# Performance work log

Measured on AMD Instinct MI355X. Metric: run time of the kernel, lower is better.

## Reference

```python
import jax, jax.numpy as jnp
import numpy as np

IN_FEATURES = 4096
OUT_FEATURES = 11008
BATCH = 64


def setup_inputs() -> dict:
    key = jax.random.key(0)
    k_x, k_w, k_s, k_b = jax.random.split(key, 4)
    x = jax.random.normal(k_x, (BATCH, IN_FEATURES), dtype=jnp.float32)
    # int8-range quantized weights stored as int8 (symmetric, [-128, 127])
    weight_q = jax.random.randint(k_w, (OUT_FEATURES, IN_FEATURES), -128, 128, dtype=jnp.int8)
    # per-output-row scales, strictly positive (absmax/127 style)
    scale = jax.random.uniform(k_s, (OUT_FEATURES, 1), dtype=jnp.float32, minval=1e-4, maxval=2e-2)
    bias = jax.random.normal(k_b, (OUT_FEATURES,), dtype=jnp.float32)
    return {"x": x, "weight_q": weight_q, "scale": scale, "bias": bias}


def reference(x, weight_q, scale, bias):
    # on-the-fly dequantization: w_deq[o, i] = weight_q[o, i] * scale[o]
    w_deq = weight_q.astype(x.dtype) * scale.astype(x.dtype)  # [O, I]
    # F.linear: y = x @ w_deq.T + bias
    return jnp.einsum('bi,oi->bo', x, w_deq) + bias
```

## Files before the change

### kernel.cpp

```cpp
#include <hip/hip_runtime.h>

#define IN_F 4096
#define OUT_F 11008
#define BATCH 64
#define NT (OUT_F / 16)
#define NWAVE 8
#define SPW (IN_F / 64 / NWAVE)

typedef int v4i __attribute__((ext_vector_type(4)));
typedef signed char i8;

__device__ __forceinline__ int pack4(int a0, int a1, int a2, int a3) {
    return (a0 & 0xff) | ((a1 & 0xff) << 8) | ((a2 & 0xff) << 16) |
           ((unsigned)a3 << 24);
}

__global__ __launch_bounds__(256)
void quant_x_kernel(const float* __restrict__ x, i8* __restrict__ xq,
                    float* __restrict__ xscale)
{
    const int b = blockIdx.x;
    const int t = threadIdx.x;
    const float* xr = x + (size_t)b * IN_F;
    const int i0 = t * 16;

    float vals[16];
    float m = 0.0f;
#pragma unroll
    for (int j = 0; j < 16; ++j) {
        vals[j] = xr[i0 + j];
        m = fmaxf(m, fabsf(vals[j]));
    }

    __shared__ float red[256];
    red[t] = m;
    __syncthreads();
    for (int s = 128; s > 0; s >>= 1) {
        if (t < s) red[t] = fmaxf(red[t], red[t + s]);
        __syncthreads();
    }
    const float amax = red[0];
    const float inv = (amax > 0.0f) ? (127.0f / amax) : 0.0f;
    if (t == 0) xscale[b] = (amax > 0.0f) ? (amax / 127.0f) : 1.0f;

    const int kc   = i0 >> 6;
    const int quad = (i0 >> 4) & 3;
    const int mt   = b >> 4;
    const int lane = (b & 15) | (quad << 4);

    i8 q[16];
#pragma unroll
    for (int j = 0; j < 16; ++j) {
        float r = rintf(vals[j] * inv);
        r = fminf(127.0f, fmaxf(-127.0f, r));
        q[j] = (i8)(int)r;
    }
    *(v4i*)(xq + ((size_t)(kc * 256 + mt * 64 + lane) * 16)) = *(const v4i*)q;
}

__global__ __launch_bounds__(512)
void gemm_kernel(const int* __restrict__ wq, const i8* __restrict__ xq,
                 const float* __restrict__ xscale,
                 const float* __restrict__ wscale,
                 const float* __restrict__ bias,
                 float* __restrict__ out)
{
    __shared__ int lds[NWAVE * 1088];
    const int lane = threadIdx.x & 63;
    const int wave = threadIdx.x >> 6;
    const int nt   = blockIdx.x;
    int* wlds = lds + wave * 1088;

    const int n    = lane & 15;
    const int q    = lane >> 4;
    const int grow = lane >> 4;
    const int gcol = (lane & 15) * 4;

    const int s0 = wave * SPW;
    const int* wbase = wq + (size_t)(nt * 16) * IN_F + s0 * 64 + gcol;
    const v4i* pA = (const v4i*)xq + (size_t)s0 * 256 + lane;

    v4i acc[4];
#pragma unroll
    for (int mt = 0; mt < 4; ++mt) acc[mt] = (v4i){0, 0, 0, 0};

    v4i wC[4], wN[4], aC[4], aN[4];
#pragma unroll
    for (int p = 0; p < 4; ++p)
        wC[p] = *(const v4i*)(wbase + (size_t)(4 * p + grow) * IN_F);
#pragma unroll
    for (int mt = 0; mt < 4; ++mt) aC[mt] = pA[mt * 64];

#pragma unroll
    for (int ss = 0; ss < SPW; ++ss) {
        if (ss + 1 < SPW) {
            const int* nb = wbase + (ss + 1) * 64;
#pragma unroll
            for (int p = 0; p < 4; ++p)
                wN[p] = *(const v4i*)(nb + (size_t)(4 * p + grow) * IN_F);
#pragma unroll
            for (int mt = 0; mt < 4; ++mt)
                aN[mt] = pA[(ss + 1) * 256 + mt * 64];
        }
#pragma unroll
        for (int p = 0; p < 4; ++p)
            *(v4i*)(wlds + (4 * p + grow) * 68 + gcol) = wC[p];
        v4i rd[4];
#pragma unroll
        for (int d = 0; d < 4; ++d)
            rd[d] = *(const v4i*)(wlds + n * 68 + q * 16 + 4 * d);

        v4i bfrag;
#pragma unroll
        for (int d = 0; d < 4; ++d)
            bfrag[d] = pack4(rd[d][0], rd[d][1], rd[d][2], rd[d][3]);

#pragma unroll
        for (int mt = 0; mt < 4; ++mt)
            acc[mt] = __builtin_amdgcn_mfma_i32_16x16x64_i8(aC[mt], bfrag, acc[mt], 0, 0, 0);

        if (ss + 1 < SPW) {
#pragma unroll
            for (int p = 0; p < 4; ++p) wC[p] = wN[p];
#pragma unroll
            for (int mt = 0; mt < 4; ++mt) aC[mt] = aN[mt];
        }
    }

#pragma unroll
    for (int mt = 0; mt < 4; ++mt)
#pragma unroll
        for (int r = 0; r < 4; ++r)
            wlds[lane * 17 + mt * 4 + r] = acc[mt][r];
    __syncthreads();

    const int mt2 = wave >> 1;
    const int rp  = (wave & 1) * 2;
    const int o   = nt * 16 + n;
    const float wsc = wscale[o];
    const float bo  = bias[o];
#pragma unroll
    for (int j = 0; j < 2; ++j) {
        const int r = rp + j;
        int s = 0;
#pragma unroll
        for (int w = 0; w < NWAVE; ++w)
            s += lds[w * 1088 + lane * 17 + mt2 * 4 + r];
        const int b = mt2 * 16 + q * 4 + r;
        out[(size_t)b * OUT_F + o] = (float)s * xscale[b] * wsc + bo;
    }
}

extern "C" void kernel_launch(void* const* d_in, const int* in_sizes, int n_in,
                              void* d_out, int out_size, void* d_ws, size_t ws_size,
                              hipStream_t stream)
{
    const float* x      = (const float*)d_in[0];
    const int*   wq     = (const int*)d_in[1];
    const float* wscale = (const float*)d_in[2];
    const float* bias   = (const float*)d_in[3];
    float* out = (float*)d_out;

    i8*    xq     = (i8*)d_ws;
    float* xscale = (float*)((char*)d_ws + 256u * 1024u);

    quant_x_kernel<<<BATCH, 256, 0, stream>>>(x, xq, xscale);
    gemm_kernel<<<NT, 512, 0, stream>>>(wq, xq, xscale, wscale, bias, out);
}
```

Before: 261.8 us.

## Stream weights directly into swizzled LDS with global_load_lds double buffering

Weight tiles now go straight from global memory into a per-wave double-buffered LDS region through global_load_lds, using an XOR swizzle, instead of passing through registers and a padded LDS store. Manual vmcnt/lgkmcnt waits order the async loads against the LDS reads. The goal is to cut VGPR pressure and the register-to-LDS store traffic in the weight-bound GEMV-like loop, and launch bounds ask for higher occupancy. The x-quantization reduction also switches to wave shuffles. The hand-written waitcnt counts are fragile, and LDS use per block grows to 64KB, which may limit how many blocks fit per CU.

```diff
diff --git a/kernel.cpp b/kernel.cpp
--- a/kernel.cpp
+++ b/kernel.cpp
@@ -13,6 +13,12 @@
 __device__ __forceinline__ int pack4(int a0, int a1, int a2, int a3) {
     return (a0 & 0xff) | ((a1 & 0xff) << 8) | ((a2 & 0xff) << 16) |
            ((unsigned)a3 << 24);
+}
+
+__device__ __forceinline__ void gload16(const int* g, int* l) {
+    __builtin_amdgcn_global_load_lds(
+        (const __attribute__((address_space(1))) void*)g,
+        (__attribute__((address_space(3))) void*)l, 16, 0, 0);
 }
 
 __global__ __launch_bounds__(256)
@@ -32,14 +38,13 @@
         m = fmaxf(m, fabsf(vals[j]));
     }
 
-    __shared__ float red[256];
-    red[t] = m;
+#pragma unroll
+    for (int o = 32; o > 0; o >>= 1) m = fmaxf(m, __shfl_xor(m, o));
+    __shared__ float wm[4];
+    if ((t & 63) == 0) wm[t >> 6] = m;
     __syncthreads();
-    for (int s = 128; s > 0; s >>= 1) {
-        if (t < s) red[t] = fmaxf(red[t], red[t + s]);
-        __syncthreads();
-    }
-    const float amax = red[0];
+    const float amax = fmaxf(fmaxf(wm[0], wm[1]), fmaxf(wm[2], wm[3]));
+
     const float inv = (amax > 0.0f) ? (127.0f / amax) : 0.0f;
     if (t == 0) xscale[b] = (amax > 0.0f) ? (amax / 127.0f) : 1.0f;
 
@@ -58,57 +63,76 @@
     *(v4i*)(xq + ((size_t)(kc * 256 + mt * 64 + lane) * 16)) = *(const v4i*)q;
 }
 
-__global__ __launch_bounds__(512)
+__global__ __launch_bounds__(512, 4)
 void gemm_kernel(const int* __restrict__ wq, const i8* __restrict__ xq,
                  const float* __restrict__ xscale,
                  const float* __restrict__ wscale,
                  const float* __restrict__ bias,
                  float* __restrict__ out)
 {
-    __shared__ int lds[NWAVE * 1088];
+    __shared__ int lds[NWAVE * 2048];
     const int lane = threadIdx.x & 63;
     const int wave = threadIdx.x >> 6;
     const int nt   = blockIdx.x;
-    int* wlds = lds + wave * 1088;
+    int* wbuf = lds + wave * 2048;
 
     const int n    = lane & 15;
     const int q    = lane >> 4;
     const int grow = lane >> 4;
-    const int gcol = (lane & 15) * 4;
+    const int col  = lane & 15;
 
     const int s0 = wave * SPW;
-    const int* wbase = wq + (size_t)(nt * 16) * IN_F + s0 * 64 + gcol;
+    const int ce = (col ^ grow) << 2;
+    const int co = (col ^ grow ^ 4) << 2;
+    const int* gbase = wq + (size_t)(nt * 16 + grow) * IN_F + s0 * 64;
+
     const v4i* pA = (const v4i*)xq + (size_t)s0 * 256 + lane;
 
     v4i acc[4];
 #pragma unroll
     for (int mt = 0; mt < 4; ++mt) acc[mt] = (v4i){0, 0, 0, 0};
 
-    v4i wC[4], wN[4], aC[4], aN[4];
+    v4i aC[4], aN[4];
+
+    int roff[4];
+#pragma unroll
+    for (int d = 0; d < 4; ++d)
+        roff[d] = n * 64 + ((((q * 4 + d) ^ (n & 7))) << 2);
+
 #pragma unroll
     for (int p = 0; p < 4; ++p)
-        wC[p] = *(const v4i*)(wbase + (size_t)(4 * p + grow) * IN_F);
+        gload16(gbase + (size_t)(4 * p) * IN_F + ((p & 1) ? co : ce),
+                wbuf + p * 256);
+    asm volatile("" ::: "memory");
 #pragma unroll
     for (int mt = 0; mt < 4; ++mt) aC[mt] = pA[mt * 64];
+    asm volatile("" ::: "memory");
 
 #pragma unroll
     for (int ss = 0; ss < SPW; ++ss) {
+        const int* cur = wbuf + (ss & 1) * 1024;
         if (ss + 1 < SPW) {
-            const int* nb = wbase + (ss + 1) * 64;
+            int* nxt = wbuf + ((ss + 1) & 1) * 1024;
+            const int* gs = gbase + (ss + 1) * 64;
 #pragma unroll
             for (int p = 0; p < 4; ++p)
-                wN[p] = *(const v4i*)(nb + (size_t)(4 * p + grow) * IN_F);
+                gload16(gs + (size_t)(4 * p) * IN_F + ((p & 1) ? co : ce),
+                        nxt + p * 256);
+            asm volatile("" ::: "memory");
 #pragma unroll
             for (int mt = 0; mt < 4; ++mt)
                 aN[mt] = pA[(ss + 1) * 256 + mt * 64];
+            asm volatile("" ::: "memory");
+            asm volatile("s_waitcnt vmcnt(12)" ::: "memory");
+        } else {
+            asm volatile("s_waitcnt vmcnt(4)" ::: "memory");
         }
-#pragma unroll
-        for (int p = 0; p < 4; ++p)
-            *(v4i*)(wlds + (4 * p + grow) * 68 + gcol) = wC[p];
+
         v4i rd[4];
 #pragma unroll
         for (int d = 0; d < 4; ++d)
-            rd[d] = *(const v4i*)(wlds + n * 68 + q * 16 + 4 * d);
+            rd[d] = *(const v4i*)(cur + roff[d]);
+        asm volatile("s_waitcnt lgkmcnt(0)" ::: "memory");
 
         v4i bfrag;
 #pragma unroll
@@ -117,21 +141,21 @@
 
 #pragma unroll
         for (int mt = 0; mt < 4; ++mt)
-            acc[mt] = __builtin_amdgcn_mfma_i32_16x16x64_i8(aC[mt], bfrag, acc[mt], 0, 0, 0);
+            acc[mt] = __builtin_amdgcn_mfma_i32_16x16x64_i8(aC[mt], bfrag,
+                                                            acc[mt], 0, 0, 0);
 
         if (ss + 1 < SPW) {
-#pragma unroll
-            for (int p = 0; p < 4; ++p) wC[p] = wN[p];
 #pragma unroll
             for (int mt = 0; mt < 4; ++mt) aC[mt] = aN[mt];
         }
     }
 
+    __syncthreads();
 #pragma unroll
     for (int mt = 0; mt < 4; ++mt)
 #pragma unroll
         for (int r = 0; r < 4; ++r)
-            wlds[lane * 17 + mt * 4 + r] = acc[mt][r];
+            lds[wave * 1088 + lane * 17 + mt * 4 + r] = acc[mt][r];
     __syncthreads();
 
     const int mt2 = wave >> 1;
```

Measured after the change: 258.9 us. Within noise of the previous version (-1.1%).

## Pack weights before LDS and double-buffer with two-stage prefetch in GEMM

Applied to the files above, without the earlier changes.

The weight tile is now packed from int32 to int8 before the LDS store, so each lane reads one 16-byte fragment instead of four, and the per-step unpack is removed. A double-buffered LDS slot holds the next step's packed weights while global loads run two steps ahead, aiming to hide memory latency behind the MFMAs. The quantize kernel's tree reduction is replaced with wave shuffles and one barrier, and the GEMM gets a launch-bounds occupancy hint. The extra prefetch stage holds more registers live, and the LDS buffers rely on each wave's own ordering with no barrier inside the loop.

```diff
diff --git a/kernel.cpp b/kernel.cpp
--- a/kernel.cpp
+++ b/kernel.cpp
@@ -32,14 +32,13 @@
         m = fmaxf(m, fabsf(vals[j]));
     }
 
-    __shared__ float red[256];
-    red[t] = m;
+#pragma unroll
+    for (int o = 32; o > 0; o >>= 1) m = fmaxf(m, __shfl_xor(m, o));
+    __shared__ float wm[4];
+    if ((t & 63) == 0) wm[t >> 6] = m;
     __syncthreads();
-    for (int s = 128; s > 0; s >>= 1) {
-        if (t < s) red[t] = fmaxf(red[t], red[t + s]);
-        __syncthreads();
-    }
-    const float amax = red[0];
+    const float amax = fmaxf(fmaxf(wm[0], wm[1]), fmaxf(wm[2], wm[3]));
+
     const float inv = (amax > 0.0f) ? (127.0f / amax) : 0.0f;
     if (t == 0) xscale[b] = (amax > 0.0f) ? (amax / 127.0f) : 1.0f;
 
@@ -58,7 +57,7 @@
     *(v4i*)(xq + ((size_t)(kc * 256 + mt * 64 + lane) * 16)) = *(const v4i*)q;
 }
 
-__global__ __launch_bounds__(512)
+__global__ __launch_bounds__(512, 4)
 void gemm_kernel(const int* __restrict__ wq, const i8* __restrict__ xq,
                  const float* __restrict__ xscale,
                  const float* __restrict__ wscale,
@@ -69,69 +68,80 @@
     const int lane = threadIdx.x & 63;
     const int wave = threadIdx.x >> 6;
     const int nt   = blockIdx.x;
-    int* wlds = lds + wave * 1088;
+    int* wbuf = lds + wave * 512;
 
     const int n    = lane & 15;
     const int q    = lane >> 4;
     const int grow = lane >> 4;
-    const int gcol = (lane & 15) * 4;
+    const int col  = lane & 15;
 
     const int s0 = wave * SPW;
-    const int* wbase = wq + (size_t)(nt * 16) * IN_F + s0 * 64 + gcol;
+    const int* gbase = wq + (size_t)(nt * 16 + grow) * IN_F + s0 * 64 + col * 4;
     const v4i* pA = (const v4i*)xq + (size_t)s0 * 256 + lane;
+
+    const int wdst = grow * 16 + col;
+    const int roff = n * 16 + q * 4;
 
     v4i acc[4];
 #pragma unroll
     for (int mt = 0; mt < 4; ++mt) acc[mt] = (v4i){0, 0, 0, 0};
 
-    v4i wC[4], wN[4], aC[4], aN[4];
+    v4i wB[4], aC[4], aN[4];
+
 #pragma unroll
     for (int p = 0; p < 4; ++p)
-        wC[p] = *(const v4i*)(wbase + (size_t)(4 * p + grow) * IN_F);
+        wB[p] = *(const v4i*)(gbase + (size_t)(4 * p) * IN_F);
 #pragma unroll
     for (int mt = 0; mt < 4; ++mt) aC[mt] = pA[mt * 64];
+#pragma unroll
+    for (int p = 0; p < 4; ++p)
+        wbuf[p * 64 + wdst] = pack4(wB[p][0], wB[p][1], wB[p][2], wB[p][3]);
+#pragma unroll
+    for (int p = 0; p < 4; ++p)
+        wB[p] = *(const v4i*)(gbase + 64 + (size_t)(4 * p) * IN_F);
+#pragma unroll
+    for (int mt = 0; mt < 4; ++mt) aN[mt] = pA[256 + mt * 64];
 
 #pragma unroll
     for (int ss = 0; ss < SPW; ++ss) {
+        v4i bfrag = *(const v4i*)(wbuf + (ss & 1) * 256 + roff);
+
         if (ss + 1 < SPW) {
-            const int* nb = wbase + (ss + 1) * 64;
+            int* dst = wbuf + ((ss + 1) & 1) * 256;
 #pragma unroll
             for (int p = 0; p < 4; ++p)
-                wN[p] = *(const v4i*)(nb + (size_t)(4 * p + grow) * IN_F);
+                dst[p * 64 + wdst] =
+                    pack4(wB[p][0], wB[p][1], wB[p][2], wB[p][3]);
+            if (ss + 2 < SPW) {
+                const int* gs = gbase + (ss + 2) * 64;
 #pragma unroll
-            for (int mt = 0; mt < 4; ++mt)
-                aN[mt] = pA[(ss + 1) * 256 + mt * 64];
+                for (int p = 0; p < 4; ++p)
+                    wB[p] = *(const v4i*)(gs + (size_t)(4 * p) * IN_F);
+            }
         }
-#pragma unroll
-        for (int p = 0; p < 4; ++p)
-            *(v4i*)(wlds + (4 * p + grow) * 68 + gcol) = wC[p];
-        v4i rd[4];
-#pragma unroll
-        for (int d = 0; d < 4; ++d)
-            rd[d] = *(const v4i*)(wlds + n * 68 + q * 16 + 4 * d);
-
-        v4i bfrag;
-#pragma unroll
-        for (int d = 0; d < 4; ++d)
-            bfrag[d] = pack4(rd[d][0], rd[d][1], rd[d][2], rd[d][3]);
 
 #pragma unroll
         for (int mt = 0; mt < 4; ++mt)
-            acc[mt] = __builtin_amdgcn_mfma_i32_16x16x64_i8(aC[mt], bfrag, acc[mt], 0, 0, 0);
+            acc[mt] = __builtin_amdgcn_mfma_i32_16x16x64_i8(aC[mt], bfrag,
+                                                            acc[mt], 0, 0, 0);
 
         if (ss + 1 < SPW) {
 #pragma unroll
-            for (int p = 0; p < 4; ++p) wC[p] = wN[p];
+            for (int mt = 0; mt < 4; ++mt) aC[mt] = aN[mt];
+            if (ss + 2 < SPW) {
 #pragma unroll
-            for (int mt = 0; mt < 4; ++mt) aC[mt] = aN[mt];
+                for (int mt = 0; mt < 4; ++mt)
+                    aN[mt] = pA[(ss + 2) * 256 + mt * 64];
+            }
         }
     }
 
+    __syncthreads();
 #pragma unroll
     for (int mt = 0; mt < 4; ++mt)
 #pragma unroll
         for (int r = 0; r < 4; ++r)
-            wlds[lane * 17 + mt * 4 + r] = acc[mt][r];
+            lds[wave * 1088 + lane * 17 + mt * 4 + r] = acc[mt][r];
     __syncthreads();
 
     const int mt2 = wave >> 1;
```

New measurement: 258.4 us. Within noise of the previous version (-1.3%).
